# Kernel tuning notes

Measured on AMD Instinct MI355X. Metric: run time of the kernel, lower is better.

The kernel has to match this reference:

```python
import jax, jax.numpy as jnp
import numpy as np

N = 50000      # nodes
E = 800000     # edges (before self loops)
IN = 128       # in_channels
HID = 128      # hidden_dim
HEADS = 4
DH = HID // HEADS  # 32 per-head dim
OUT = 32       # out_channels
NEG_SLOPE = 0.2


def setup_inputs() -> dict:
    key = jax.random.key(0)
    ks = jax.random.split(key, 20)
    s = 0.05
    inp = {}
    inp["x"] = jax.random.normal(ks[0], (N, IN), jnp.float32)
    inp["current_node_idx"] = jax.random.randint(ks[1], (1024,), 0, N, dtype=jnp.int32)
    inp["edge_index"] = jax.random.randint(ks[2], (2, E), 0, N, dtype=jnp.int32)
    # input linear
    inp["W_in"] = jax.random.normal(ks[3], (IN, HID), jnp.float32) * s
    inp["b_in"] = jnp.zeros((HID,), jnp.float32)
    # residual linear
    inp["W_res"] = jax.random.normal(ks[4], (HID, HID), jnp.float32) * s
    inp["b_res"] = jnp.zeros((HID,), jnp.float32)
    # GAT layer 1
    inp["W_g1"] = jax.random.normal(ks[5], (HID, HID), jnp.float32) * s
    inp["a_src1"] = jax.random.normal(ks[6], (HEADS, DH), jnp.float32) * s
    inp["a_dst1"] = jax.random.normal(ks[7], (HEADS, DH), jnp.float32) * s
    inp["b_g1"] = jnp.zeros((HID,), jnp.float32)
    # GAT layer 2
    inp["W_g2"] = jax.random.normal(ks[8], (HID, HID), jnp.float32) * s
    inp["a_src2"] = jax.random.normal(ks[9], (HEADS, DH), jnp.float32) * s
    inp["a_dst2"] = jax.random.normal(ks[10], (HEADS, DH), jnp.float32) * s
    inp["b_g2"] = jnp.zeros((HID,), jnp.float32)
    # output MLP
    inp["W_o1"] = jax.random.normal(ks[11], (HID, HID // 2), jnp.float32) * s
    inp["b_o1"] = jnp.zeros((HID // 2,), jnp.float32)
    inp["W_o2"] = jax.random.normal(ks[12], (HID // 2, OUT), jnp.float32) * s
    inp["b_o2"] = jnp.zeros((OUT,), jnp.float32)
    return inp


def gat_conv(x, src, dst, W, a_src, a_dst, bias):
    """PyG GATConv (concat heads, add_self_loops already in src/dst), eval mode."""
    xp = (x @ W).reshape(-1, HEADS, DH)              # [N, H, D]
    e_src = jnp.einsum('nhd,hd->nh', xp, a_src)      # [N, H]
    e_dst = jnp.einsum('nhd,hd->nh', xp, a_dst)      # [N, H]
    e = jax.nn.leaky_relu(e_src[src] + e_dst[dst], NEG_SLOPE)  # [E', H]
    m = jax.ops.segment_max(e, dst, num_segments=N)  # per-dst max (self loops guarantee nonempty)
    w = jnp.exp(e - m[dst])
    z = jax.ops.segment_sum(w, dst, num_segments=N)
    alpha = w / z[dst]                               # [E', H]
    msg = alpha[:, :, None] * xp[src]                # [E', H, D]
    out = jax.ops.segment_sum(msg, dst, num_segments=N)  # [N, H, D]
    return out.reshape(-1, HID) + bias


def reference(x, current_node_idx, edge_index, W_in, b_in, W_res, b_res,
              W_g1, a_src1, a_dst1, b_g1, W_g2, a_src2, a_dst2, b_g2,
              W_o1, b_o1, W_o2, b_o2):
    # add self loops (PyG GATConv default)
    loops = jnp.arange(N, dtype=edge_index.dtype)
    src = jnp.concatenate([edge_index[0], loops])
    dst = jnp.concatenate([edge_index[1], loops])

    h = jax.nn.relu(x @ W_in + b_in)                 # dropout = identity (eval)
    residual = h @ W_res + b_res
    h = jax.nn.relu(gat_conv(h, src, dst, W_g1, a_src1, a_dst1, b_g1))
    h = jax.nn.relu(gat_conv(h, src, dst, W_g2, a_src2, a_dst2, b_g2))
    h = h + residual
    emb = h[current_node_idx]                        # [B, HID]
    out = jax.nn.relu(emb @ W_o1 + b_o1) @ W_o2 + b_o2
    return out
```

## Files before the change

### kernel.cpp

```cpp
#include <hip/hip_runtime.h>
#include <hip/hip_bf16.h>
#include <hip/hip_fp16.h>
#include <math.h>

#define HID 128
#define HEADS 4
#define DH 32
#define NEG_SLOPE 0.2f


__global__ void hist_k(const int* __restrict__ ei, int E, int EP,
                       int* __restrict__ counts, int* __restrict__ rank) {
    int e = blockIdx.x * 256 + threadIdx.x;
    if (e >= EP) return;
    int d = (e < E) ? ei[E + e] : (e - E);
    rank[e] = atomicAdd(counts + d, 1);
}

__global__ __launch_bounds__(1024) void scan_block_k(const int* __restrict__ counts,
                                                     int* __restrict__ offs,
                                                     int* __restrict__ bsums, int n) {
    __shared__ int tmp[1024];
    int tid = threadIdx.x;
    int g = blockIdx.x * 1024 + tid;
    int v = (g < n) ? counts[g] : 0;
    tmp[tid] = v;
    __syncthreads();
    for (int off = 1; off < 1024; off <<= 1) {
        int t = (tid >= off) ? tmp[tid - off] : 0;
        __syncthreads();
        tmp[tid] += t;
        __syncthreads();
    }
    if (g < n) offs[g] = tmp[tid] - v;
    if (tid == 1023) bsums[blockIdx.x] = tmp[1023];
}

__global__ void scan_tops_k(int* __restrict__ bsums, int nb, int* __restrict__ offs,
                            int n, int total) {
    int l = threadIdx.x;
    int v = (l < nb) ? bsums[l] : 0;
    int orig = v;
    for (int d = 1; d < 64; d <<= 1) {
        int t = __shfl_up(v, d, 64);
        if (l >= d) v += t;
    }
    if (l < nb) bsums[l] = v - orig;
    if (l == 0) offs[n] = total;
}

__global__ void scan_add_k(int* __restrict__ offs, const int* __restrict__ bsums, int n) {
    int g = blockIdx.x * 256 + threadIdx.x;
    if (g < n) offs[g] += bsums[g >> 10];
}

__global__ void scatter_k(const int* __restrict__ ei, int E, int EP,
                          const int* __restrict__ offs, const int* __restrict__ rank,
                          int* __restrict__ ssrc) {
    int e = blockIdx.x * 256 + threadIdx.x;
    if (e >= EP) return;
    int s, d;
    if (e < E) { s = ei[e]; d = ei[E + e]; } else { s = d = e - E; }
    ssrc[offs[d] + rank[e]] = s;
}


#define XSPAD 132

template<int RELU, int BIAS>
__global__ __launch_bounds__(256) void gemm128_k(const float* __restrict__ X,
                                                 const float* __restrict__ W,
                                                 const float* __restrict__ bias,
                                                 float* __restrict__ Y, int nrows) {
    __shared__ float xs[128][XSPAD];
    const int tid = threadIdx.x;
    const int rowbase = blockIdx.x * 128;

    {
        const float4* Xv = reinterpret_cast<const float4*>(X + (size_t)rowbase * HID);
#pragma unroll
        for (int i = 0; i < 16; ++i) {
            int ii = tid + i * 256;
            int r = ii >> 5;
            int c4 = ii & 31;
            float4 v = make_float4(0.f, 0.f, 0.f, 0.f);
            if (rowbase + r < nrows) v = Xv[ii];
            *reinterpret_cast<float4*>(&xs[r][c4 * 4]) = v;
        }
    }
    __syncthreads();

    const int ct = (tid & 15) * 8;
    const int rt = (tid >> 4) * 8;
    float4 accA[8], accB[8];
#pragma unroll
    for (int i = 0; i < 8; ++i) {
        accA[i] = make_float4(0.f, 0.f, 0.f, 0.f);
        accB[i] = make_float4(0.f, 0.f, 0.f, 0.f);
    }
    const float* Wp = W + ct;

#pragma unroll 2
    for (int k = 0; k < HID; k += 4) {
        float4 xr[8];
#pragma unroll
        for (int i = 0; i < 8; ++i) xr[i] = *reinterpret_cast<const float4*>(&xs[rt + i][k]);
#pragma unroll
        for (int j = 0; j < 4; ++j) {
            float4 w0 = *reinterpret_cast<const float4*>(Wp + (size_t)(k + j) * HID);
            float4 w1 = *reinterpret_cast<const float4*>(Wp + (size_t)(k + j) * HID + 4);
#pragma unroll
            for (int i = 0; i < 8; ++i) {
                float xi = (j == 0) ? xr[i].x : (j == 1) ? xr[i].y : (j == 2) ? xr[i].z : xr[i].w;
                accA[i].x += xi * w0.x; accA[i].y += xi * w0.y;
                accA[i].z += xi * w0.z; accA[i].w += xi * w0.w;
                accB[i].x += xi * w1.x; accB[i].y += xi * w1.y;
                accB[i].z += xi * w1.z; accB[i].w += xi * w1.w;
            }
        }
    }

    float4 bv0 = make_float4(0,0,0,0), bv1 = bv0;
    if (BIAS) {
        bv0 = *reinterpret_cast<const float4*>(bias + ct);
        bv1 = *reinterpret_cast<const float4*>(bias + ct + 4);
    }
#pragma unroll
    for (int i = 0; i < 8; ++i) {
        int r = rowbase + rt + i;
        if (r < nrows) {
            float4 a = accA[i], b = accB[i];
            a.x += bv0.x; a.y += bv0.y; a.z += bv0.z; a.w += bv0.w;
            b.x += bv1.x; b.y += bv1.y; b.z += bv1.z; b.w += bv1.w;
            if (RELU) {
                a.x = fmaxf(a.x, 0.f); a.y = fmaxf(a.y, 0.f);
                a.z = fmaxf(a.z, 0.f); a.w = fmaxf(a.w, 0.f);
                b.x = fmaxf(b.x, 0.f); b.y = fmaxf(b.y, 0.f);
                b.z = fmaxf(b.z, 0.f); b.w = fmaxf(b.w, 0.f);
            }
            *reinterpret_cast<float4*>(Y + (size_t)r * HID + ct) = a;
            *reinterpret_cast<float4*>(Y + (size_t)r * HID + ct + 4) = b;
        }
    }
}


__global__ __launch_bounds__(256) void gemm_gat_k(const float* __restrict__ X,
                                                  const float* __restrict__ W,
                                                  const float* __restrict__ a_src,
                                                  const float* __restrict__ a_dst,
                                                  __half* __restrict__ XPH,
                                                  float* __restrict__ es,
                                                  float* __restrict__ ed, int nrows) {
    __shared__ float xs[128][XSPAD];
    const int tid = threadIdx.x;
    const int rowbase = blockIdx.x * 128;

    {
        const float4* Xv = reinterpret_cast<const float4*>(X + (size_t)rowbase * HID);
#pragma unroll
        for (int i = 0; i < 16; ++i) {
            int ii = tid + i * 256;
            int r = ii >> 5;
            int c4 = ii & 31;
            float4 v = make_float4(0.f, 0.f, 0.f, 0.f);
            if (rowbase + r < nrows) v = Xv[ii];
            *reinterpret_cast<float4*>(&xs[r][c4 * 4]) = v;
        }
    }
    __syncthreads();

    const int ct = (tid & 15) * 8;
    const int rt = (tid >> 4) * 8;
    float4 accA[8], accB[8];
#pragma unroll
    for (int i = 0; i < 8; ++i) {
        accA[i] = make_float4(0.f, 0.f, 0.f, 0.f);
        accB[i] = make_float4(0.f, 0.f, 0.f, 0.f);
    }
    const float* Wp = W + ct;

#pragma unroll 2
    for (int k = 0; k < HID; k += 4) {
        float4 xr[8];
#pragma unroll
        for (int i = 0; i < 8; ++i) xr[i] = *reinterpret_cast<const float4*>(&xs[rt + i][k]);
#pragma unroll
        for (int j = 0; j < 4; ++j) {
            float4 w0 = *reinterpret_cast<const float4*>(Wp + (size_t)(k + j) * HID);
            float4 w1 = *reinterpret_cast<const float4*>(Wp + (size_t)(k + j) * HID + 4);
#pragma unroll
            for (int i = 0; i < 8; ++i) {
                float xi = (j == 0) ? xr[i].x : (j == 1) ? xr[i].y : (j == 2) ? xr[i].z : xr[i].w;
                accA[i].x += xi * w0.x; accA[i].y += xi * w0.y;
                accA[i].z += xi * w0.z; accA[i].w += xi * w0.w;
                accB[i].x += xi * w1.x; accB[i].y += xi * w1.y;
                accB[i].z += xi * w1.z; accB[i].w += xi * w1.w;
            }
        }
    }

    const float4 av0 = *reinterpret_cast<const float4*>(a_src + ct);
    const float4 av1 = *reinterpret_cast<const float4*>(a_src + ct + 4);
    const float4 dv0 = *reinterpret_cast<const float4*>(a_dst + ct);
    const float4 dv1 = *reinterpret_cast<const float4*>(a_dst + ct + 4);
#pragma unroll
    for (int i = 0; i < 8; ++i) {
        int r = rowbase + rt + i;
        float4 a = accA[i], b = accB[i];
        float ps = a.x * av0.x + a.y * av0.y + a.z * av0.z + a.w * av0.w
                 + b.x * av1.x + b.y * av1.y + b.z * av1.z + b.w * av1.w;
        float pd = a.x * dv0.x + a.y * dv0.y + a.z * dv0.z + a.w * dv0.w
                 + b.x * dv1.x + b.y * dv1.y + b.z * dv1.z + b.w * dv1.w;
        ps += __shfl_xor(ps, 1); ps += __shfl_xor(ps, 2);
        pd += __shfl_xor(pd, 1); pd += __shfl_xor(pd, 2);
        if (r < nrows) {
            __half2 p0 = __floats2half2_rn(a.x, a.y);
            __half2 p1 = __floats2half2_rn(a.z, a.w);
            __half2 p2 = __floats2half2_rn(b.x, b.y);
            __half2 p3 = __floats2half2_rn(b.z, b.w);
            uint4 u;
            u.x = *reinterpret_cast<unsigned int*>(&p0);
            u.y = *reinterpret_cast<unsigned int*>(&p1);
            u.z = *reinterpret_cast<unsigned int*>(&p2);
            u.w = *reinterpret_cast<unsigned int*>(&p3);
            *reinterpret_cast<uint4*>(XPH + (size_t)r * HID + ct) = u;
            if ((tid & 3) == 0) {
                int h = (tid & 15) >> 2;
                es[r * HEADS + h] = ps;
                ed[r * HEADS + h] = pd;
            }
        }
    }
}


#define LEAKY(v) ((v) > 0.f ? (v) : NEG_SLOPE * (v))

template<bool ADDRES>
__global__ __launch_bounds__(256) void aggregate_k(const __half* __restrict__ xph,
                                                   const float* __restrict__ esrc,
                                                   const float* __restrict__ edst,
                                                   const int* __restrict__ offs,
                                                   const int* __restrict__ ssrc,
                                                   const float* __restrict__ bias,
                                                   const float* __restrict__ res,
                                                   float* __restrict__ out, int n) {
    int n0 = blockIdx.x * 4 + (threadIdx.x >> 6);
    if (n0 >= n) return;
    int lane = threadIdx.x & 63;
    int h = lane >> 4;
    int c2 = lane * 2;
    int beg = offs[n0], end = offs[n0 + 1];
    float ed = edst[n0 * HEADS + h];

    float zs = 0.f, acc0 = 0.f, acc1 = 0.f;

    int e = beg;
    for (; e + 8 <= end; e += 8) {
        int s[8];
#pragma unroll
        for (int q = 0; q < 8; ++q) s[q] = ssrc[e + q];
        __half2 hx[8];
#pragma unroll
        for (int q = 0; q < 8; ++q)
            hx[q] = reinterpret_cast<const __half2*>(xph + (size_t)s[q] * HID)[lane];
        float wv[8];
#pragma unroll
        for (int q = 0; q < 8; ++q) {
            float v = esrc[s[q] * HEADS + h] + ed;
            v = LEAKY(v);
            wv[q] = __expf(v);
        }
#pragma unroll
        for (int q = 0; q < 8; ++q) {
            float2 xv = __half22float2(hx[q]);
            zs += wv[q];
            acc0 += wv[q] * xv.x;
            acc1 += wv[q] * xv.y;
        }
    }
    for (; e < end; ++e) {
        int s = ssrc[e];
        __half2 hv = reinterpret_cast<const __half2*>(xph + (size_t)s * HID)[lane];
        float v = esrc[s * HEADS + h] + ed;
        v = LEAKY(v);
        float w = __expf(v);
        float2 xv = __half22float2(hv);
        zs += w;
        acc0 += w * xv.x;
        acc1 += w * xv.y;
    }

    float inv = 1.0f / zs;
    float o0 = fmaxf(acc0 * inv + bias[c2], 0.f);
    float o1 = fmaxf(acc1 * inv + bias[c2 + 1], 0.f);
    if (ADDRES) {
        o0 += res[(size_t)n0 * HID + c2];
        o1 += res[(size_t)n0 * HID + c2 + 1];
    }
    out[(size_t)n0 * HID + c2] = o0;
    out[(size_t)n0 * HID + c2 + 1] = o1;
}


__global__ __launch_bounds__(64) void mlp_k(const float* __restrict__ h,
                                            const int* __restrict__ idx,
                                            const float* __restrict__ W1,
                                            const float* __restrict__ b1,
                                            const float* __restrict__ W2,
                                            const float* __restrict__ b2,
                                            float* __restrict__ out) {
    __shared__ float emb[128];
    __shared__ float t[64];
    int b = blockIdx.x, l = threadIdx.x;
    int n = idx[b];
    *reinterpret_cast<float2*>(&emb[l * 2]) =
        *reinterpret_cast<const float2*>(&h[(size_t)n * HID + l * 2]);
    __syncthreads();
    float acc = b1[l];
#pragma unroll
    for (int k = 0; k < 128; ++k) acc += emb[k] * W1[k * 64 + l];
    t[l] = fmaxf(acc, 0.f);
    __syncthreads();
    if (l < 32) {
        float o = b2[l];
#pragma unroll
        for (int k = 0; k < 64; ++k) o += t[k] * W2[k * 32 + l];
        out[b * 32 + l] = o;
    }
}


extern "C" void kernel_launch(void* const* d_in, const int* in_sizes, int n_in,
                              void* d_out, int out_size, void* d_ws, size_t ws_size,
                              hipStream_t stream) {
    const float* x      = (const float*)d_in[0];
    const int*   cni    = (const int*)  d_in[1];
    const int*   ei     = (const int*)  d_in[2];
    const float* W_in   = (const float*)d_in[3];
    const float* b_in   = (const float*)d_in[4];
    const float* W_res  = (const float*)d_in[5];
    const float* b_res  = (const float*)d_in[6];
    const float* W_g1   = (const float*)d_in[7];
    const float* a_src1 = (const float*)d_in[8];
    const float* a_dst1 = (const float*)d_in[9];
    const float* b_g1   = (const float*)d_in[10];
    const float* W_g2   = (const float*)d_in[11];
    const float* a_src2 = (const float*)d_in[12];
    const float* a_dst2 = (const float*)d_in[13];
    const float* b_g2   = (const float*)d_in[14];
    const float* W_o1   = (const float*)d_in[15];
    const float* b_o1   = (const float*)d_in[16];
    const float* W_o2   = (const float*)d_in[17];
    const float* b_o2   = (const float*)d_in[18];

    const int N  = in_sizes[0] / HID;
    const int B  = in_sizes[1];
    const int E  = in_sizes[2] / 2;
    const int EP = E + N;

    char* w = (char*)d_ws;
    auto alloc = [&](size_t bytes) {
        char* p = w;
        w += (bytes + 255) & ~(size_t)255;
        return p;
    };
    float*  h      = (float*) alloc((size_t)N * HID * 4);
    float*  res    = (float*) alloc((size_t)N * HID * 4);
    __half* xph    = (__half*)alloc((size_t)N * HID * 2);
    float*  esrc   = (float*) alloc((size_t)N * HEADS * 4);
    float*  edst   = (float*) alloc((size_t)N * HEADS * 4);
    int*    counts = (int*)   alloc((size_t)N * 4);
    int*    offs   = (int*)   alloc((size_t)(N + 1) * 4);
    int*    bsums  = (int*)   alloc(256 * 4);
    int*    rank   = (int*)   alloc((size_t)EP * 4);
    int*    ssrc   = (int*)   alloc((size_t)EP * 4);

    hipMemsetAsync(counts, 0, (size_t)N * 4, stream);
    hist_k<<<(EP + 255) / 256, 256, 0, stream>>>(ei, E, EP, counts, rank);
    int NB = (N + 1023) / 1024;
    scan_block_k<<<NB, 1024, 0, stream>>>(counts, offs, bsums, N);
    scan_tops_k<<<1, 64, 0, stream>>>(bsums, NB, offs, N, EP);
    scan_add_k<<<(N + 255) / 256, 256, 0, stream>>>(offs, bsums, N);
    scatter_k<<<(EP + 255) / 256, 256, 0, stream>>>(ei, E, EP, offs, rank, ssrc);

    int gb = (N + 127) / 128;
    gemm128_k<1, 1><<<gb, 256, 0, stream>>>(x, W_in, b_in, h, N);
    gemm128_k<0, 1><<<gb, 256, 0, stream>>>(h, W_res, b_res, res, N);
    gemm_gat_k<<<gb, 256, 0, stream>>>(h, W_g1, a_src1, a_dst1, xph, esrc, edst, N);
    aggregate_k<false><<<(N + 3) / 4, 256, 0, stream>>>(xph, esrc, edst, offs, ssrc,
                                                        b_g1, nullptr, h, N);
    gemm_gat_k<<<gb, 256, 0, stream>>>(h, W_g2, a_src2, a_dst2, xph, esrc, edst, N);
    aggregate_k<true><<<(N + 3) / 4, 256, 0, stream>>>(xph, esrc, edst, offs, ssrc,
                                                       b_g2, res, h, N);
    mlp_k<<<B, 64, 0, stream>>>(h, cni, W_o1, b_o1, W_o2, b_o2, (float*)d_out);
}
```

Before: 371.4 us.

## Use fp16 MFMA for residual and GAT GEMMs with half-precision activations

Three of the four dense 128x128 GEMMs (residual and both GAT projections) move from fp32 FMA code to fp16 MFMA 16x16x32 instructions, with W converted and transposed into LDS per block. Intermediate activations (input-layer output and layer-1 aggregation output) are now stored as fp16, which halves their memory traffic and feeds the MFMA A fragments directly. The cost is lower precision in the projections, a per-block weight staging pass, and uncoalesced scalar half stores for XPH.

Result: faster. 334.4 us (-10.0%).

```diff
diff --git a/kernel.cpp b/kernel.cpp
--- a/kernel.cpp
+++ b/kernel.cpp
@@ -7,6 +7,10 @@
 #define HEADS 4
 #define DH 32
 #define NEG_SLOPE 0.2f
+
+typedef _Float16 half8_t __attribute__((ext_vector_type(8)));
+typedef float f32x4_t __attribute__((ext_vector_type(4)));
+union H8 { half8_t v; uint2 u[2]; };
 
 
 __global__ void hist_k(const int* __restrict__ ei, int E, int EP,
@@ -67,11 +71,10 @@
 
 #define XSPAD 132
 
-template<int RELU, int BIAS>
-__global__ __launch_bounds__(256) void gemm128_k(const float* __restrict__ X,
+__global__ __launch_bounds__(256) void gemm_in_k(const float* __restrict__ X,
                                                  const float* __restrict__ W,
                                                  const float* __restrict__ bias,
-                                                 float* __restrict__ Y, int nrows) {
+                                                 __half* __restrict__ Y, int nrows) {
     __shared__ float xs[128][XSPAD];
     const int tid = threadIdx.x;
     const int rowbase = blockIdx.x * 128;
@@ -120,101 +123,17 @@
         }
     }
 
-    float4 bv0 = make_float4(0,0,0,0), bv1 = bv0;
-    if (BIAS) {
-        bv0 = *reinterpret_cast<const float4*>(bias + ct);
-        bv1 = *reinterpret_cast<const float4*>(bias + ct + 4);
-    }
+    float4 bv0 = *reinterpret_cast<const float4*>(bias + ct);
+    float4 bv1 = *reinterpret_cast<const float4*>(bias + ct + 4);
 #pragma unroll
     for (int i = 0; i < 8; ++i) {
         int r = rowbase + rt + i;
         if (r < nrows) {
             float4 a = accA[i], b = accB[i];
-            a.x += bv0.x; a.y += bv0.y; a.z += bv0.z; a.w += bv0.w;
-            b.x += bv1.x; b.y += bv1.y; b.z += bv1.z; b.w += bv1.w;
-            if (RELU) {
-                a.x = fmaxf(a.x, 0.f); a.y = fmaxf(a.y, 0.f);
-                a.z = fmaxf(a.z, 0.f); a.w = fmaxf(a.w, 0.f);
-                b.x = fmaxf(b.x, 0.f); b.y = fmaxf(b.y, 0.f);
-                b.z = fmaxf(b.z, 0.f); b.w = fmaxf(b.w, 0.f);
-            }
-            *reinterpret_cast<float4*>(Y + (size_t)r * HID + ct) = a;
-            *reinterpret_cast<float4*>(Y + (size_t)r * HID + ct + 4) = b;
-        }
-    }
-}
-
-
-__global__ __launch_bounds__(256) void gemm_gat_k(const float* __restrict__ X,
-                                                  const float* __restrict__ W,
-                                                  const float* __restrict__ a_src,
-                                                  const float* __restrict__ a_dst,
-                                                  __half* __restrict__ XPH,
-                                                  float* __restrict__ es,
-                                                  float* __restrict__ ed, int nrows) {
-    __shared__ float xs[128][XSPAD];
-    const int tid = threadIdx.x;
-    const int rowbase = blockIdx.x * 128;
-
-    {
-        const float4* Xv = reinterpret_cast<const float4*>(X + (size_t)rowbase * HID);
-#pragma unroll
-        for (int i = 0; i < 16; ++i) {
-            int ii = tid + i * 256;
-            int r = ii >> 5;
-            int c4 = ii & 31;
-            float4 v = make_float4(0.f, 0.f, 0.f, 0.f);
-            if (rowbase + r < nrows) v = Xv[ii];
-            *reinterpret_cast<float4*>(&xs[r][c4 * 4]) = v;
-        }
-    }
-    __syncthreads();
-
-    const int ct = (tid & 15) * 8;
-    const int rt = (tid >> 4) * 8;
-    float4 accA[8], accB[8];
-#pragma unroll
-    for (int i = 0; i < 8; ++i) {
-        accA[i] = make_float4(0.f, 0.f, 0.f, 0.f);
-        accB[i] = make_float4(0.f, 0.f, 0.f, 0.f);
-    }
-    const float* Wp = W + ct;
-
-#pragma unroll 2
-    for (int k = 0; k < HID; k += 4) {
-        float4 xr[8];
-#pragma unroll
-        for (int i = 0; i < 8; ++i) xr[i] = *reinterpret_cast<const float4*>(&xs[rt + i][k]);
-#pragma unroll
-        for (int j = 0; j < 4; ++j) {
-            float4 w0 = *reinterpret_cast<const float4*>(Wp + (size_t)(k + j) * HID);
-            float4 w1 = *reinterpret_cast<const float4*>(Wp + (size_t)(k + j) * HID + 4);
-#pragma unroll
-            for (int i = 0; i < 8; ++i) {
-                float xi = (j == 0) ? xr[i].x : (j == 1) ? xr[i].y : (j == 2) ? xr[i].z : xr[i].w;
-                accA[i].x += xi * w0.x; accA[i].y += xi * w0.y;
-                accA[i].z += xi * w0.z; accA[i].w += xi * w0.w;
-                accB[i].x += xi * w1.x; accB[i].y += xi * w1.y;
-                accB[i].z += xi * w1.z; accB[i].w += xi * w1.w;
-            }
-        }
-    }
-
-    const float4 av0 = *reinterpret_cast<const float4*>(a_src + ct);
-    const float4 av1 = *reinterpret_cast<const float4*>(a_src + ct + 4);
-    const float4 dv0 = *reinterpret_cast<const float4*>(a_dst + ct);
-    const float4 dv1 = *reinterpret_cast<const float4*>(a_dst + ct + 4);
-#pragma unroll
-    for (int i = 0; i < 8; ++i) {
-        int r = rowbase + rt + i;
-        float4 a = accA[i], b = accB[i];
-        float ps = a.x * av0.x + a.y * av0.y + a.z * av0.z + a.w * av0.w
-                 + b.x * av1.x + b.y * av1.y + b.z * av1.z + b.w * av1.w;
-        float pd = a.x * dv0.x + a.y * dv0.y + a.z * dv0.z + a.w * dv0.w
-                 + b.x * dv1.x + b.y * dv1.y + b.z * dv1.z + b.w * dv1.w;
-        ps += __shfl_xor(ps, 1); ps += __shfl_xor(ps, 2);
-        pd += __shfl_xor(pd, 1); pd += __shfl_xor(pd, 2);
-        if (r < nrows) {
+            a.x = fmaxf(a.x + bv0.x, 0.f); a.y = fmaxf(a.y + bv0.y, 0.f);
+            a.z = fmaxf(a.z + bv0.z, 0.f); a.w = fmaxf(a.w + bv0.w, 0.f);
+            b.x = fmaxf(b.x + bv1.x, 0.f); b.y = fmaxf(b.y + bv1.y, 0.f);
+            b.z = fmaxf(b.z + bv1.z, 0.f); b.w = fmaxf(b.w + bv1.w, 0.f);
             __half2 p0 = __floats2half2_rn(a.x, a.y);
             __half2 p1 = __floats2half2_rn(a.z, a.w);
             __half2 p2 = __floats2half2_rn(b.x, b.y);
@@ -224,20 +143,152 @@
             u.y = *reinterpret_cast<unsigned int*>(&p1);
             u.z = *reinterpret_cast<unsigned int*>(&p2);
             u.w = *reinterpret_cast<unsigned int*>(&p3);
-            *reinterpret_cast<uint4*>(XPH + (size_t)r * HID + ct) = u;
-            if ((tid & 3) == 0) {
-                int h = (tid & 15) >> 2;
+            *reinterpret_cast<uint4*>(Y + (size_t)r * HID + ct) = u;
+        }
+    }
+}
+
+
+#define WTPAD 132
+
+__device__ inline void stage_wt(const float* __restrict__ W, __half* wt, int tid) {
+    for (int it = 0; it < 64; ++it) {
+        int lin = it * 256 + tid;
+        int k = lin >> 7, n = lin & 127;
+        wt[n * WTPAD + k] = __float2half(W[lin]);
+    }
+}
+
+__device__ inline void load_afrags(const __half* __restrict__ A16, int m, int g,
+                                   int nrows, half8_t* a) {
+    if (m < nrows) {
+        const __half* hp = A16 + (size_t)m * HID;
+#pragma unroll
+        for (int kb = 0; kb < 4; ++kb) {
+            H8 t;
+            t.u[0] = *reinterpret_cast<const uint2*>(hp + kb * 32 + g * 4);
+            t.u[1] = *reinterpret_cast<const uint2*>(hp + kb * 32 + g * 4 + 16);
+            a[kb] = t.v;
+        }
+    } else {
+#pragma unroll
+        for (int kb = 0; kb < 4; ++kb) {
+            H8 t; t.u[0] = make_uint2(0u, 0u); t.u[1] = make_uint2(0u, 0u);
+            a[kb] = t.v;
+        }
+    }
+}
+
+
+__global__ __launch_bounds__(256) void gemm_res_mfma_k(const __half* __restrict__ A16,
+                                                       const float* __restrict__ W,
+                                                       const float* __restrict__ bias,
+                                                       float* __restrict__ Y, int nrows) {
+    __shared__ __half wt[128 * WTPAD];
+    const int tid = threadIdx.x;
+    stage_wt(W, wt, tid);
+    __syncthreads();
+
+    const int lane = tid & 63;
+    const int wid = tid >> 6;
+    const int c = lane & 15;
+    const int g = lane >> 4;
+    const int row0 = blockIdx.x * 64 + wid * 16;
+
+    half8_t a[4];
+    load_afrags(A16, row0 + c, g, nrows, a);
+
+#pragma unroll
+    for (int t = 0; t < 8; ++t) {
+        f32x4_t acc = {0.f, 0.f, 0.f, 0.f};
+        const __half* wp = &wt[(t * 16 + c) * WTPAD];
+#pragma unroll
+        for (int kb = 0; kb < 4; ++kb) {
+            H8 b;
+            b.u[0] = *reinterpret_cast<const uint2*>(wp + kb * 32 + g * 4);
+            b.u[1] = *reinterpret_cast<const uint2*>(wp + kb * 32 + g * 4 + 16);
+            acc = __builtin_amdgcn_mfma_f32_16x16x32_f16(a[kb], b.v, acc, 0, 0, 0);
+        }
+        float bcol = bias[t * 16 + c];
+#pragma unroll
+        for (int i = 0; i < 4; ++i) {
+            int r = row0 + g * 4 + i;
+            if (r < nrows) Y[(size_t)r * HID + t * 16 + c] = acc[i] + bcol;
+        }
+    }
+}
+
+
+__global__ __launch_bounds__(256) void gemm_gat_mfma_k(const __half* __restrict__ A16,
+                                                       const float* __restrict__ W,
+                                                       const float* __restrict__ a_src,
+                                                       const float* __restrict__ a_dst,
+                                                       __half* __restrict__ XPH,
+                                                       float* __restrict__ es,
+                                                       float* __restrict__ ed, int nrows) {
+    __shared__ __half wt[128 * WTPAD];
+    const int tid = threadIdx.x;
+    stage_wt(W, wt, tid);
+    __syncthreads();
+
+    const int lane = tid & 63;
+    const int wid = tid >> 6;
+    const int c = lane & 15;
+    const int g = lane >> 4;
+    const int row0 = blockIdx.x * 64 + wid * 16;
+
+    half8_t a[4];
+    load_afrags(A16, row0 + c, g, nrows, a);
+
+    float as[8], ad[8];
+#pragma unroll
+    for (int t = 0; t < 8; ++t) { as[t] = a_src[t * 16 + c]; ad[t] = a_dst[t * 16 + c]; }
+
+    f32x4_t acc[8];
+#pragma unroll
+    for (int t = 0; t < 8; ++t) {
+        f32x4_t z = {0.f, 0.f, 0.f, 0.f};
+        const __half* wp = &wt[(t * 16 + c) * WTPAD];
+#pragma unroll
+        for (int kb = 0; kb < 4; ++kb) {
+            H8 b;
+            b.u[0] = *reinterpret_cast<const uint2*>(wp + kb * 32 + g * 4);
+            b.u[1] = *reinterpret_cast<const uint2*>(wp + kb * 32 + g * 4 + 16);
+            z = __builtin_amdgcn_mfma_f32_16x16x32_f16(a[kb], b.v, z, 0, 0, 0);
+        }
+        acc[t] = z;
+    }
+
+#pragma unroll
+    for (int t = 0; t < 8; ++t)
+#pragma unroll
+        for (int i = 0; i < 4; ++i) {
+            int r = row0 + g * 4 + i;
+            if (r < nrows) XPH[(size_t)r * HID + t * 16 + c] = __float2half(acc[t][i]);
+        }
+
+#pragma unroll
+    for (int h = 0; h < 4; ++h)
+#pragma unroll
+        for (int i = 0; i < 4; ++i) {
+            float ps = acc[2 * h][i] * as[2 * h] + acc[2 * h + 1][i] * as[2 * h + 1];
+            float pd = acc[2 * h][i] * ad[2 * h] + acc[2 * h + 1][i] * ad[2 * h + 1];
+            ps += __shfl_xor(ps, 1); ps += __shfl_xor(ps, 2);
+            ps += __shfl_xor(ps, 4); ps += __shfl_xor(ps, 8);
+            pd += __shfl_xor(pd, 1); pd += __shfl_xor(pd, 2);
+            pd += __shfl_xor(pd, 4); pd += __shfl_xor(pd, 8);
+            int r = row0 + g * 4 + i;
+            if (c == 0 && r < nrows) {
                 es[r * HEADS + h] = ps;
                 ed[r * HEADS + h] = pd;
             }
         }
-    }
 }
 
 
 #define LEAKY(v) ((v) > 0.f ? (v) : NEG_SLOPE * (v))
 
-template<bool ADDRES>
+template<bool ADDRES, bool OUTH>
 __global__ __launch_bounds__(256) void aggregate_k(const __half* __restrict__ xph,
                                                    const float* __restrict__ esrc,
                                                    const float* __restrict__ edst,
@@ -245,7 +296,8 @@
                                                    const int* __restrict__ ssrc,
                                                    const float* __restrict__ bias,
                                                    const float* __restrict__ res,
-                                                   float* __restrict__ out, int n) {
+                                                   float* __restrict__ outf,
+                                                   __half* __restrict__ outh, int n) {
     int n0 = blockIdx.x * 4 + (threadIdx.x >> 6);
     if (n0 >= n) return;
     int lane = threadIdx.x & 63;
@@ -299,8 +351,12 @@
         o0 += res[(size_t)n0 * HID + c2];
         o1 += res[(size_t)n0 * HID + c2 + 1];
     }
-    out[(size_t)n0 * HID + c2] = o0;
-    out[(size_t)n0 * HID + c2 + 1] = o1;
+    if (OUTH) {
+        *reinterpret_cast<__half2*>(outh + (size_t)n0 * HID + c2) = __floats2half2_rn(o0, o1);
+    } else {
+        outf[(size_t)n0 * HID + c2] = o0;
+        outf[(size_t)n0 * HID + c2 + 1] = o1;
+    }
 }
 
 
@@ -366,7 +422,9 @@
         w += (bytes + 255) & ~(size_t)255;
         return p;
     };
-    float*  h      = (float*) alloc((size_t)N * HID * 4);
+    __half* h16a   = (__half*)alloc((size_t)N * HID * 2);
+    __half* h16b   = (__half*)alloc((size_t)N * HID * 2);
+    float*  hf     = (float*) alloc((size_t)N * HID * 4);
     float*  res    = (float*) alloc((size_t)N * HID * 4);
     __half* xph    = (__half*)alloc((size_t)N * HID * 2);
     float*  esrc   = (float*) alloc((size_t)N * HEADS * 4);
@@ -385,14 +443,15 @@
     scan_add_k<<<(N + 255) / 256, 256, 0, stream>>>(offs, bsums, N);
     scatter_k<<<(EP + 255) / 256, 256, 0, stream>>>(ei, E, EP, offs, rank, ssrc);
 
-    int gb = (N + 127) / 128;
-    gemm128_k<1, 1><<<gb, 256, 0, stream>>>(x, W_in, b_in, h, N);
-    gemm128_k<0, 1><<<gb, 256, 0, stream>>>(h, W_res, b_res, res, N);
-    gemm_gat_k<<<gb, 256, 0, stream>>>(h, W_g1, a_src1, a_dst1, xph, esrc, edst, N);
-    aggregate_k<false><<<(N + 3) / 4, 256, 0, stream>>>(xph, esrc, edst, offs, ssrc,
-                                                        b_g1, nullptr, h, N);
-    gemm_gat_k<<<gb, 256, 0, stream>>>(h, W_g2, a_src2, a_dst2, xph, esrc, edst, N);
-    aggregate_k<true><<<(N + 3) / 4, 256, 0, stream>>>(xph, esrc, edst, offs, ssrc,
-                                                       b_g2, res, h, N);
-    mlp_k<<<B, 64, 0, stream>>>(h, cni, W_o1, b_o1, W_o2, b_o2, (float*)d_out);
-}
+    int gin = (N + 127) / 128;
+    int gmf = (N + 63) / 64;
+    gemm_in_k<<<gin, 256, 0, stream>>>(x, W_in, b_in, h16a, N);
+    gemm_res_mfma_k<<<gmf, 256, 0, stream>>>(h16a, W_res, b_res, res, N);
+    gemm_gat_mfma_k<<<gmf, 256, 0, stream>>>(h16a, W_g1, a_src1, a_dst1, xph, esrc, edst, N);
+    aggregate_k<false, true><<<(N + 3) / 4, 256, 0, stream>>>(xph, esrc, edst, offs, ssrc,
+                                                              b_g1, nullptr, nullptr, h16b, N);
+    gemm_gat_mfma_k<<<gmf, 256, 0, stream>>>(h16b, W_g2, a_src2, a_dst2, xph, esrc, edst, N);
+    aggregate_k<true, false><<<(N + 3) / 4, 256, 0, stream>>>(xph, esrc, edst, offs, ssrc,
+                                                              b_g2, res, hf, nullptr, N);
+    mlp_k<<<B, 64, 0, stream>>>(hf, cni, W_o1, b_o1, W_o2, b_o2, (float*)d_out);
+}
```
